# Optimization experiments

Hardware: AMD Instinct MI355X
Metric: run time of the kernel (lower is better)

The kernel has to match this reference:

```python
import jax, jax.numpy as jnp
import numpy as np

DIM = 256
HEADS = 8
WIN = 64
SHIFT = 32
HIDDEN = 1024  # dim * mlp_ratio
EPS = 1e-5


def layernorm(x, g, b):
    mu = jnp.mean(x, axis=-1, keepdims=True)
    var = jnp.mean(jnp.square(x - mu), axis=-1, keepdims=True)
    return (x - mu) * jax.lax.rsqrt(var + EPS) * g + b


def setup_inputs() -> dict:
    key = jax.random.key(0)
    ks = jax.random.split(key, 12)
    B, L = 8, 16384
    s = lambda fan: 1.0 / np.sqrt(fan)
    return {
        "x": jax.random.normal(ks[0], (B, L, DIM), dtype=jnp.float32),
        "g1": jnp.ones((DIM,), jnp.float32),
        "b1": jnp.zeros((DIM,), jnp.float32),
        "qkv_w": jax.random.normal(ks[1], (DIM, 3 * DIM), jnp.float32) * s(DIM),
        "qkv_b": jnp.zeros((3 * DIM,), jnp.float32),
        "rpb_table": jax.random.normal(ks[2], (2 * WIN - 1, HEADS), jnp.float32) * 0.02,
        "proj_w": jax.random.normal(ks[3], (DIM, DIM), jnp.float32) * s(DIM),
        "proj_b": jnp.zeros((DIM,), jnp.float32),
        "g2": jnp.ones((DIM,), jnp.float32),
        "b2": jnp.zeros((DIM,), jnp.float32),
        "fc1_w": jax.random.normal(ks[4], (DIM, HIDDEN), jnp.float32) * s(DIM),
        "fc1_b": jnp.zeros((HIDDEN,), jnp.float32),
        "fc2_w": jax.random.normal(ks[5], (HIDDEN, DIM), jnp.float32) * s(HIDDEN),
        "fc2_b": jnp.zeros((DIM,), jnp.float32),
    }


def reference(x, g1, b1, qkv_w, qkv_b, rpb_table, proj_w, proj_b, g2, b2, fc1_w, fc1_b, fc2_w, fc2_b):
    B, L, C = x.shape
    hd = C // HEADS
    scale = hd ** (-0.5)

    shortcut = x
    xn = layernorm(x, g1, b1)

    # shift: roll left, zero wrapped-around tail (faithful to original in-place zeroing)
    shifted = jnp.roll(xn, -SHIFT, axis=1)
    shifted = shifted.at[:, -SHIFT:].set(0.0)

    nW = L // WIN
    xw = shifted.reshape(B * nW, WIN, C)

    # qkv projection
    qkv = xw @ qkv_w + qkv_b
    qkv = qkv.reshape(-1, WIN, 3, HEADS, hd).transpose(2, 0, 3, 1, 4)
    q, k, v = qkv[0], qkv[1], qkv[2]

    attn = jnp.einsum('bhnd,bhmd->bhnm', q * scale, k)

    idx = jnp.arange(WIN)
    rel = idx[:, None] - idx[None, :] + (WIN - 1)
    bias = rpb_table[rel].transpose(2, 0, 1)
    attn = attn + bias[None]

    attn = jax.nn.softmax(attn, axis=-1)
    out = jnp.einsum('bhnm,bhmd->bhnd', attn, v)
    out = out.transpose(0, 2, 1, 3).reshape(-1, WIN, C)
    out = out @ proj_w + proj_b

    # window reverse + unshift (zero wrapped head, faithful to original)
    xr = out.reshape(B, L, C)
    xr = jnp.roll(xr, SHIFT, axis=1)
    xr = xr.at[:, :SHIFT].set(0.0)

    x1 = shortcut + xr
    h = layernorm(x1, g2, b2)
    h = jax.nn.gelu(h @ fc1_w + fc1_b, approximate=False)
    h = h @ fc2_w + fc2_b
    return x1 + h
```

## Files before the change

### kernel.cpp

```cpp
#include <hip/hip_runtime.h>
#include <hip/hip_bf16.h>
#include <stdint.h>

#define LSEQ   16384
#define NBATCH 8
#define MROWS  (NBATCH*LSEQ)
#define CDIM   256
#define NHEADS 8
#define HDIM   32
#define NWIN   64
#define NSH    32
#define NHID   1024

typedef unsigned short u16;
typedef __attribute__((ext_vector_type(4))) float f32x4;
typedef __attribute__((ext_vector_type(8))) short s16x8;

__device__ __forceinline__ u16 f2bf(float f) {
  union { float f; unsigned u; } c; c.f = f;
  unsigned r = c.u + 0x7FFFu + ((c.u >> 16) & 1u);
  return (u16)(r >> 16);
}

__device__ __forceinline__ float gelu_fast(float v) {
  float t = v * v;
  float u2 = v * fmaf(t, 0.0713548162726f, 1.59576912161f);
  float e = __expf(u2);
  float r = __builtin_amdgcn_rcpf(e + 1.f);
  return fmaf(-v, r, v);
}

__global__ __launch_bounds__(256) void wtrans_kernel(const float* __restrict__ in,
                                                     u16* __restrict__ out, int K, int N) {
  __shared__ float tile[64][65];
  int k0 = blockIdx.x * 64, n0 = blockIdx.y * 64;
  int t = threadIdx.x;
  int r = t >> 4, cb = (t & 15) * 4;
#pragma unroll
  for (int p = 0; p < 4; ++p) {
    const float4 v = *(const float4*)(in + (size_t)(k0 + r + p*16) * N + n0 + cb);
    tile[r+p*16][cb+0] = v.x; tile[r+p*16][cb+1] = v.y;
    tile[r+p*16][cb+2] = v.z; tile[r+p*16][cb+3] = v.w;
  }
  __syncthreads();
#pragma unroll
  for (int p = 0; p < 4; ++p) {
    int nl = r + p*16;
    ushort4 o;
    o.x = f2bf(tile[cb+0][nl]); o.y = f2bf(tile[cb+1][nl]);
    o.z = f2bf(tile[cb+2][nl]); o.w = f2bf(tile[cb+3][nl]);
    *(ushort4*)(out + (size_t)(n0+nl)*K + k0 + cb) = o;
  }
}

__global__ __launch_bounds__(256) void ln_shift_kernel(const float* __restrict__ x,
                                                       const float* __restrict__ g,
                                                       const float* __restrict__ b,
                                                       u16* __restrict__ out) {
  int row  = blockIdx.x * 4 + (threadIdx.x >> 6);
  int lane = threadIdx.x & 63;
  u16* op = out + (size_t)row * CDIM + lane*4;
  int l  = row & (LSEQ-1);
  int ls = l + NSH;
  if (ls >= LSEQ) { *(ushort4*)op = make_ushort4(0,0,0,0); return; }
  const float4 v = *(const float4*)(x + ((size_t)(row - l) + ls) * CDIM + lane*4);
  float s  = v.x+v.y+v.z+v.w;
  float s2 = v.x*v.x + v.y*v.y + v.z*v.z + v.w*v.w;
#pragma unroll
  for (int m = 1; m < 64; m <<= 1) { s += __shfl_xor(s, m); s2 += __shfl_xor(s2, m); }
  float mean = s * (1.f/CDIM);
  float rs = rsqrtf(s2*(1.f/CDIM) - mean*mean + 1e-5f);
  const float4 gv = *(const float4*)(g + lane*4);
  const float4 bv = *(const float4*)(b + lane*4);
  ushort4 o;
  o.x = f2bf((v.x-mean)*rs*gv.x + bv.x);
  o.y = f2bf((v.y-mean)*rs*gv.y + bv.y);
  o.z = f2bf((v.z-mean)*rs*gv.z + bv.z);
  o.w = f2bf((v.w-mean)*rs*gv.w + bv.w);
  *(ushort4*)op = o;
}

template<int KDIM, int NDIM, int EPI>
__global__ __launch_bounds__(256) void gemm_kernel(const u16* __restrict__ A,
                                                   const u16* __restrict__ BT,
                                                   const float* __restrict__ bias,
                                                   void* __restrict__ Cout,
                                                   const float* __restrict__ res) {
  __shared__ __align__(16) u16 As[128*64];
  __shared__ __align__(16) u16 Bs[128*64];
  const int t = threadIdx.x, wave = t >> 6, lane = t & 63;
  constexpr int NT_N = NDIM / 128;
  constexpr int G = 32;
  const int bid = blockIdx.x;
  const int chunk = bid / (G * NT_N);
  const int rem = bid - chunk * (G * NT_N);
  const int tn = rem / G;
  const int tm = chunk * G + (rem - tn * G);
  f32x4 acc[4][4];
#pragma unroll
  for (int m = 0; m < 4; ++m)
#pragma unroll
    for (int n = 0; n < 4; ++n) acc[m][n] = (f32x4){0.f,0.f,0.f,0.f};

  const size_t Aoff = (size_t)tm * 128 * KDIM;
  const size_t Boff = (size_t)tn * 128 * KDIM;
  int rowS[4], kblkS[4];
#pragma unroll
  for (int p = 0; p < 4; ++p) {
    int i = p*256 + t; rowS[p] = i >> 3;
    kblkS[p] = ((i & 7) ^ (rowS[p] & 7)) * 8;
  }
  const int wr = (wave >> 1) * 64, wc = (wave & 1) * 64;

  for (int kt = 0; kt < KDIM/64; ++kt) {
    const int k0 = kt * 64;
#pragma unroll
    for (int p = 0; p < 4; ++p) {
      __builtin_amdgcn_global_load_lds(
        (const __attribute__((address_space(1))) void*)(A + Aoff + (size_t)rowS[p]*KDIM + k0 + kblkS[p]),
        (__attribute__((address_space(3))) void*)(As + (p*256 + wave*64)*8), 16, 0, 0);
      __builtin_amdgcn_global_load_lds(
        (const __attribute__((address_space(1))) void*)(BT + Boff + (size_t)rowS[p]*KDIM + k0 + kblkS[p]),
        (__attribute__((address_space(3))) void*)(Bs + (p*256 + wave*64)*8), 16, 0, 0);
    }
    asm volatile("s_waitcnt vmcnt(0)" ::: "memory");
    __syncthreads();
#pragma unroll
    for (int kk = 0; kk < 2; ++kk) {
      s16x8 af[4], bf[4];
#pragma unroll
      for (int m = 0; m < 4; ++m) {
        int r = wr + m*16 + (lane & 15);
        int slot = (kk*4 + (lane >> 4)) ^ (r & 7);
        af[m] = *(const s16x8*)&As[r*64 + slot*8];
      }
#pragma unroll
      for (int n = 0; n < 4; ++n) {
        int r = wc + n*16 + (lane & 15);
        int slot = (kk*4 + (lane >> 4)) ^ (r & 7);
        bf[n] = *(const s16x8*)&Bs[r*64 + slot*8];
      }
#pragma unroll
      for (int m = 0; m < 4; ++m)
#pragma unroll
        for (int n = 0; n < 4; ++n)
          acc[m][n] = __builtin_amdgcn_mfma_f32_16x16x32_bf16(bf[n], af[m], acc[m][n], 0, 0, 0);
    }
    __syncthreads();
  }

  const int g = lane >> 4, c0 = lane & 15;
  const size_t row0 = (size_t)tm*128 + wr;
  const int col0 = tn*128 + wc;
  float4 bvv[4];
#pragma unroll
  for (int n = 0; n < 4; ++n) bvv[n] = *(const float4*)(bias + col0 + n*16 + g*4);

  if constexpr (EPI == 0) {
    u16* out = (u16*)Cout;
#pragma unroll
    for (int m = 0; m < 4; ++m) {
      size_t R = row0 + m*16 + c0;
      u16* orow = out + R * NDIM + col0 + g*4;
#pragma unroll
      for (int n = 0; n < 4; ++n) {
        ushort4 o;
        o.x = f2bf(acc[m][n][0] + bvv[n].x);
        o.y = f2bf(acc[m][n][1] + bvv[n].y);
        o.z = f2bf(acc[m][n][2] + bvv[n].z);
        o.w = f2bf(acc[m][n][3] + bvv[n].w);
        *(ushort4*)(orow + n*16) = o;
      }
    }
  } else if constexpr (EPI == 2) {
    u16* out = (u16*)Cout;
#pragma unroll
    for (int m = 0; m < 4; ++m) {
      size_t R = row0 + m*16 + c0;
      u16* orow = out + R * NDIM + col0 + g*4;
#pragma unroll
      for (int n = 0; n < 4; ++n) {
        ushort4 o;
        o.x = f2bf(gelu_fast(acc[m][n][0] + bvv[n].x));
        o.y = f2bf(gelu_fast(acc[m][n][1] + bvv[n].y));
        o.z = f2bf(gelu_fast(acc[m][n][2] + bvv[n].z));
        o.w = f2bf(gelu_fast(acc[m][n][3] + bvv[n].w));
        *(ushort4*)(orow + n*16) = o;
      }
    }
  } else {
    float* out = (float*)Cout;
#pragma unroll
    for (int m = 0; m < 4; ++m) {
      size_t R = row0 + m*16 + c0;
      size_t base = R * NDIM + col0 + g*4;
#pragma unroll
      for (int n = 0; n < 4; ++n) {
        float4 rv = *(const float4*)(res + base + n*16);
        float4 o;
        o.x = rv.x + acc[m][n][0] + bvv[n].x;
        o.y = rv.y + acc[m][n][1] + bvv[n].y;
        o.z = rv.z + acc[m][n][2] + bvv[n].z;
        o.w = rv.w + acc[m][n][3] + bvv[n].w;
        *(float4*)(out + base + n*16) = o;
      }
    }
  }
}

__global__ __launch_bounds__(256) void proj_ln_kernel(const u16* __restrict__ A,
                                                      const u16* __restrict__ BT,
                                                      const float* __restrict__ bias,
                                                      const float* __restrict__ x,
                                                      const float* __restrict__ g2,
                                                      const float* __restrict__ b2,
                                                      float* __restrict__ out,
                                                      u16* __restrict__ ln_out) {
  __shared__ __align__(16) u16 As[64*64];
  __shared__ __align__(16) u16 Bs[256*64];
  const int t = threadIdx.x, wave = t >> 6, lane = t & 63;
  const int g = lane >> 4, c0 = lane & 15;
  const int row0 = blockIdx.x * 64;

  f32x4 acc[16];
#pragma unroll
  for (int n = 0; n < 16; ++n) acc[n] = (f32x4){0.f,0.f,0.f,0.f};

  for (int kt = 0; kt < 4; ++kt) {
    const int k0 = kt * 64;
#pragma unroll
    for (int p = 0; p < 2; ++p) {
      int i = p*256 + t;
      int r = i >> 3;
      int srow = row0 - NSH + r; if (srow < 0) srow = 0;
      int kb = ((i & 7) ^ (r & 7)) * 8;
      __builtin_amdgcn_global_load_lds(
        (const __attribute__((address_space(1))) void*)(A + (size_t)srow*CDIM + k0 + kb),
        (__attribute__((address_space(3))) void*)(As + i*8), 16, 0, 0);
    }
#pragma unroll
    for (int p = 0; p < 8; ++p) {
      int i = p*256 + t;
      int r = i >> 3;
      int kb = ((i & 7) ^ (r & 7)) * 8;
      __builtin_amdgcn_global_load_lds(
        (const __attribute__((address_space(1))) void*)(BT + (size_t)r*CDIM + k0 + kb),
        (__attribute__((address_space(3))) void*)(Bs + i*8), 16, 0, 0);
    }
    asm volatile("s_waitcnt vmcnt(0)" ::: "memory");
    __syncthreads();
#pragma unroll
    for (int kk = 0; kk < 2; ++kk) {
      const int ar = wave*16 + c0;
      s16x8 af = *(const s16x8*)&As[ar*64 + (((kk*4 + g) ^ (ar & 7)) * 8)];
#pragma unroll
      for (int nn = 0; nn < 4; ++nn) {
        s16x8 bf[4];
#pragma unroll
        for (int q = 0; q < 4; ++q) {
          int rn = (nn*4 + q)*16 + c0;
          bf[q] = *(const s16x8*)&Bs[rn*64 + (((kk*4 + g) ^ (rn & 7)) * 8)];
        }
#pragma unroll
        for (int q = 0; q < 4; ++q)
          acc[nn*4+q] = __builtin_amdgcn_mfma_f32_16x16x32_bf16(bf[q], af, acc[nn*4+q], 0, 0, 0);
      }
    }
    __syncthreads();
  }

  const int D = row0 + wave*16 + c0;
  const int l_d = D & (LSEQ-1);
  const bool addp = (l_d >= NSH);
  float s = 0.f, s2 = 0.f;
  f32x4 x1v[16];
#pragma unroll
  for (int n = 0; n < 16; ++n) {
    const int col = n*16 + g*4;
    const float4 xv = *(const float4*)(x + (size_t)D*CDIM + col);
    const float4 bv = *(const float4*)(bias + col);
    f32x4 v;
    v[0] = addp ? xv.x + acc[n][0] + bv.x : xv.x;
    v[1] = addp ? xv.y + acc[n][1] + bv.y : xv.y;
    v[2] = addp ? xv.z + acc[n][2] + bv.z : xv.z;
    v[3] = addp ? xv.w + acc[n][3] + bv.w : xv.w;
    *(f32x4*)(out + (size_t)D*CDIM + col) = v;
    x1v[n] = v;
    s  += v[0]+v[1]+v[2]+v[3];
    s2 += v[0]*v[0]+v[1]*v[1]+v[2]*v[2]+v[3]*v[3];
  }
  s  += __shfl_xor(s, 16);  s  += __shfl_xor(s, 32);
  s2 += __shfl_xor(s2, 16); s2 += __shfl_xor(s2, 32);
  const float mean = s * (1.f/CDIM);
  const float rs = rsqrtf(s2*(1.f/CDIM) - mean*mean + 1e-5f);
#pragma unroll
  for (int n = 0; n < 16; ++n) {
    const int col = n*16 + g*4;
    const float4 gv = *(const float4*)(g2 + col);
    const float4 bv = *(const float4*)(b2 + col);
    ushort4 o;
    o.x = f2bf((x1v[n][0]-mean)*rs*gv.x + bv.x);
    o.y = f2bf((x1v[n][1]-mean)*rs*gv.y + bv.y);
    o.z = f2bf((x1v[n][2]-mean)*rs*gv.z + bv.z);
    o.w = f2bf((x1v[n][3]-mean)*rs*gv.w + bv.w);
    *(ushort4*)(ln_out + (size_t)D*CDIM + col) = o;
  }
}

__global__ __launch_bounds__(256) void attn_kernel(const u16* __restrict__ qkv,
                                                   const float* __restrict__ rpb,
                                                   u16* __restrict__ out) {
  __shared__ __align__(16) u16 VT[NHEADS*HDIM*NWIN];
  __shared__ __align__(16) u16 Pl[4*NWIN*NWIN];
  __shared__ float biasl[NHEADS][128];
  const int t = threadIdx.x, wave = t >> 6, lane = t & 63;
  const int g = lane >> 4, c0 = lane & 15;
  const size_t rowbase = (size_t)blockIdx.x * NWIN;

  for (int e = t; e < NHEADS*128; e += 256) {
    int h = e >> 7, i = e & 127;
    biasl[h][i] = (i < 2*NWIN-1) ? rpb[i*NHEADS + h] : 0.f;
  }
  {
    int cA = t >> 5;
    int inner = t & 31;
    int hh = inner >> 2, d0 = (inner & 3) * 8;
#pragma unroll
    for (int p = 0; p < 8; ++p) {
      int c = p*8 + cA;
      s16x8 v = *(const s16x8*)&qkv[(rowbase + c)*768 + 512 + hh*32 + d0];
#pragma unroll
      for (int j = 0; j < 8; ++j) {
        int d = d0 + j;
        int slot = (c >> 3) ^ (d & 7) ^ hh;
        *(u16*)((char*)VT + hh*4096 + d*128 + slot*16 + (c & 7)*2) = (u16)v[j];
      }
    }
  }
  __syncthreads();

  const float scale = 0.17677669529663687f;
#pragma unroll 1
  for (int rep = 0; rep < 2; ++rep) {
    const int h = wave*2 + rep;
    s16x8 qf[4], kf[4];
#pragma unroll
    for (int m = 0; m < 4; ++m)
      qf[m] = *(const s16x8*)&qkv[(rowbase + m*16 + c0)*768 + h*32 + g*8];
#pragma unroll
    for (int n = 0; n < 4; ++n)
      kf[n] = *(const s16x8*)&qkv[(rowbase + n*16 + c0)*768 + 256 + h*32 + g*8];
    f32x4 sa[4][4];
#pragma unroll
    for (int m = 0; m < 4; ++m)
#pragma unroll
      for (int n = 0; n < 4; ++n) sa[m][n] = (f32x4){0.f,0.f,0.f,0.f};
#pragma unroll
    for (int m = 0; m < 4; ++m)
#pragma unroll
      for (int n = 0; n < 4; ++n)
        sa[m][n] = __builtin_amdgcn_mfma_f32_16x16x32_bf16(qf[m], kf[n], sa[m][n], 0, 0, 0);
#pragma unroll
    for (int m = 0; m < 4; ++m)
#pragma unroll
      for (int n = 0; n < 4; ++n) {
        int idx0 = (m-n)*16 + 4*g - c0 + 63;
#pragma unroll
        for (int j = 0; j < 4; ++j)
          sa[m][n][j] = sa[m][n][j]*scale + biasl[h][idx0 + j];
      }
    float rm[4][4], rsum[4][4];
#pragma unroll
    for (int m = 0; m < 4; ++m)
#pragma unroll
      for (int j = 0; j < 4; ++j) {
        float mx = fmaxf(fmaxf(sa[m][0][j], sa[m][1][j]), fmaxf(sa[m][2][j], sa[m][3][j]));
        mx = fmaxf(mx, __shfl_xor(mx, 1));
        mx = fmaxf(mx, __shfl_xor(mx, 2));
        mx = fmaxf(mx, __shfl_xor(mx, 4));
        mx = fmaxf(mx, __shfl_xor(mx, 8));
        rm[m][j] = mx;
      }
#pragma unroll
    for (int m = 0; m < 4; ++m)
#pragma unroll
      for (int n = 0; n < 4; ++n)
#pragma unroll
        for (int j = 0; j < 4; ++j)
          sa[m][n][j] = __expf(sa[m][n][j] - rm[m][j]);
#pragma unroll
    for (int m = 0; m < 4; ++m)
#pragma unroll
      for (int j = 0; j < 4; ++j) {
        float s = sa[m][0][j] + sa[m][1][j] + sa[m][2][j] + sa[m][3][j];
        s += __shfl_xor(s, 1);
        s += __shfl_xor(s, 2);
        s += __shfl_xor(s, 4);
        s += __shfl_xor(s, 8);
        rsum[m][j] = 1.f / s;
      }
    asm volatile("s_waitcnt lgkmcnt(0)" ::: "memory");
#pragma unroll
    for (int m = 0; m < 4; ++m)
#pragma unroll
      for (int n = 0; n < 4; ++n)
#pragma unroll
        for (int j = 0; j < 4; ++j) {
          int r = m*16 + 4*g + j, c = n*16 + c0;
          *(u16*)((char*)Pl + wave*8192 + r*128 + (((c>>3)^(r&7))*16) + (c&7)*2)
            = f2bf(sa[m][n][j] * rsum[m][j]);
        }
    asm volatile("s_waitcnt lgkmcnt(0)" ::: "memory");
    __builtin_amdgcn_sched_barrier(0);
    f32x4 oa[4][2];
#pragma unroll
    for (int m = 0; m < 4; ++m) { oa[m][0] = (f32x4){0.f,0.f,0.f,0.f}; oa[m][1] = (f32x4){0.f,0.f,0.f,0.f}; }
#pragma unroll
    for (int kk = 0; kk < 2; ++kk) {
      s16x8 pa[4], vb[2];
#pragma unroll
      for (int m = 0; m < 4; ++m) {
        int r = m*16 + c0;
        int slot = (kk*4 + g) ^ (r & 7);
        pa[m] = *(const s16x8*)((const char*)Pl + wave*8192 + r*128 + slot*16);
      }
#pragma unroll
      for (int n = 0; n < 2; ++n) {
        int d = n*16 + c0;
        int slot = (kk*4 + g) ^ (d & 7) ^ h;
        vb[n] = *(const s16x8*)((const char*)VT + h*4096 + d*128 + slot*16);
      }
#pragma unroll
      for (int m = 0; m < 4; ++m)
#pragma unroll
        for (int n = 0; n < 2; ++n)
          oa[m][n] = __builtin_amdgcn_mfma_f32_16x16x32_bf16(vb[n], pa[m], oa[m][n], 0, 0, 0);
    }
#pragma unroll
    for (int m = 0; m < 4; ++m) {
      u16* op = out + (rowbase + m*16 + c0)*CDIM + h*32 + g*4;
#pragma unroll
      for (int n = 0; n < 2; ++n) {
        ushort4 o;
        o.x = f2bf(oa[m][n][0]); o.y = f2bf(oa[m][n][1]);
        o.z = f2bf(oa[m][n][2]); o.w = f2bf(oa[m][n][3]);
        *(ushort4*)(op + n*16) = o;
      }
    }
  }
}

extern "C" void kernel_launch(void* const* d_in, const int* in_sizes, int n_in,
                              void* d_out, int out_size, void* d_ws, size_t ws_size,
                              hipStream_t stream) {
  const float* x      = (const float*)d_in[0];
  const float* g1     = (const float*)d_in[1];
  const float* b1     = (const float*)d_in[2];
  const float* qkv_w  = (const float*)d_in[3];
  const float* qkv_b  = (const float*)d_in[4];
  const float* rpb    = (const float*)d_in[5];
  const float* proj_w = (const float*)d_in[6];
  const float* proj_b = (const float*)d_in[7];
  const float* g2     = (const float*)d_in[8];
  const float* b2     = (const float*)d_in[9];
  const float* fc1_w  = (const float*)d_in[10];
  const float* fc1_b  = (const float*)d_in[11];
  const float* fc2_w  = (const float*)d_in[12];
  const float* fc2_b  = (const float*)d_in[13];
  float* out = (float*)d_out;

  u16* R0     = (u16*)d_ws;
  u16* R1     = R0 + (size_t)MROWS*768;
  u16* qkvwT  = R1 + (size_t)MROWS*1024;
  u16* projwT = qkvwT + 768*256;
  u16* fc1wT  = projwT + 256*256;
  u16* fc2wT  = fc1wT + 1024*256;

  wtrans_kernel<<<dim3(4, 12), 256, 0, stream>>>(qkv_w, qkvwT, 256, 768);
  wtrans_kernel<<<dim3(4, 4),  256, 0, stream>>>(proj_w, projwT, 256, 256);
  wtrans_kernel<<<dim3(4, 16), 256, 0, stream>>>(fc1_w, fc1wT, 256, 1024);
  wtrans_kernel<<<dim3(16, 4), 256, 0, stream>>>(fc2_w, fc2wT, 1024, 256);

  constexpr int NT_M = MROWS/128;
  ln_shift_kernel<<<MROWS/4, 256, 0, stream>>>(x, g1, b1, R1);
  gemm_kernel<256, 768, 0><<<NT_M*6, 256, 0, stream>>>(R1, qkvwT, qkv_b, R0, nullptr);
  attn_kernel<<<MROWS/NWIN, 256, 0, stream>>>(R0, rpb, R1);
  proj_ln_kernel<<<MROWS/64, 256, 0, stream>>>(R1, projwT, proj_b, x, g2, b2, out, R0);
  gemm_kernel<256, 1024, 2><<<NT_M*8, 256, 0, stream>>>(R0, fc1wT, fc1_b, R1, nullptr);
  gemm_kernel<1024, 256, 3><<<NT_M*2, 256, 0, stream>>>(R1, fc2wT, fc2_b, out, out);
}
```

Baseline: 682.4 us.

## Double-buffer LDS tiles in GEMM and proj kernels to overlap loads with MFMA

Converts the generic GEMM and the fused proj+LayerNorm kernel from a single-buffered load-wait-compute loop into a two-stage ping-pong. The next K tile is fetched into a second LDS buffer with global_load_lds while MFMAs run on the current one, which hides global memory latency. LDS use doubles, which may lower occupancy. The block-swizzle group size is also reduced for large-K GEMMs (the fc2 GEMM) to change L2 reuse.

```diff
diff --git a/kernel.cpp b/kernel.cpp
--- a/kernel.cpp
+++ b/kernel.cpp
@@ -86,11 +86,12 @@
                                                    const float* __restrict__ bias,
                                                    void* __restrict__ Cout,
                                                    const float* __restrict__ res) {
-  __shared__ __align__(16) u16 As[128*64];
-  __shared__ __align__(16) u16 Bs[128*64];
+  __shared__ __align__(16) u16 As[2][128*64];
+  __shared__ __align__(16) u16 Bs[2][128*64];
   const int t = threadIdx.x, wave = t >> 6, lane = t & 63;
   constexpr int NT_N = NDIM / 128;
-  constexpr int G = 32;
+  constexpr int G = (KDIM >= 1024) ? 8 : 32;
+  constexpr int NTK = KDIM / 64;
   const int bid = blockIdx.x;
   const int chunk = bid / (G * NT_N);
   const int rem = bid - chunk * (G * NT_N);
@@ -112,19 +113,19 @@
   }
   const int wr = (wave >> 1) * 64, wc = (wave & 1) * 64;
 
-  for (int kt = 0; kt < KDIM/64; ++kt) {
+  auto STAGE = [&](u16* AsD, u16* BsD, int kt) {
     const int k0 = kt * 64;
 #pragma unroll
     for (int p = 0; p < 4; ++p) {
       __builtin_amdgcn_global_load_lds(
         (const __attribute__((address_space(1))) void*)(A + Aoff + (size_t)rowS[p]*KDIM + k0 + kblkS[p]),
-        (__attribute__((address_space(3))) void*)(As + (p*256 + wave*64)*8), 16, 0, 0);
+        (__attribute__((address_space(3))) void*)(AsD + (p*256 + wave*64)*8), 16, 0, 0);
       __builtin_amdgcn_global_load_lds(
         (const __attribute__((address_space(1))) void*)(BT + Boff + (size_t)rowS[p]*KDIM + k0 + kblkS[p]),
-        (__attribute__((address_space(3))) void*)(Bs + (p*256 + wave*64)*8), 16, 0, 0);
-    }
-    asm volatile("s_waitcnt vmcnt(0)" ::: "memory");
-    __syncthreads();
+        (__attribute__((address_space(3))) void*)(BsD + (p*256 + wave*64)*8), 16, 0, 0);
+    }
+  };
+  auto COMPUTE = [&](const u16* AsS, const u16* BsS) {
 #pragma unroll
     for (int kk = 0; kk < 2; ++kk) {
       s16x8 af[4], bf[4];
@@ -132,13 +133,13 @@
       for (int m = 0; m < 4; ++m) {
         int r = wr + m*16 + (lane & 15);
         int slot = (kk*4 + (lane >> 4)) ^ (r & 7);
-        af[m] = *(const s16x8*)&As[r*64 + slot*8];
+        af[m] = *(const s16x8*)&AsS[r*64 + slot*8];
       }
 #pragma unroll
       for (int n = 0; n < 4; ++n) {
         int r = wc + n*16 + (lane & 15);
         int slot = (kk*4 + (lane >> 4)) ^ (r & 7);
-        bf[n] = *(const s16x8*)&Bs[r*64 + slot*8];
+        bf[n] = *(const s16x8*)&BsS[r*64 + slot*8];
       }
 #pragma unroll
       for (int m = 0; m < 4; ++m)
@@ -146,6 +147,21 @@
         for (int n = 0; n < 4; ++n)
           acc[m][n] = __builtin_amdgcn_mfma_f32_16x16x32_bf16(bf[n], af[m], acc[m][n], 0, 0, 0);
     }
+  };
+
+  STAGE(As[0], Bs[0], 0);
+  asm volatile("s_waitcnt vmcnt(0)" ::: "memory");
+  __syncthreads();
+#pragma unroll 1
+  for (int kt2 = 0; kt2 < NTK/2; ++kt2) {
+    const int kt = kt2 * 2;
+    if (kt + 1 < NTK) STAGE(As[1], Bs[1], kt + 1);
+    COMPUTE(As[0], Bs[0]);
+    asm volatile("s_waitcnt vmcnt(0)" ::: "memory");
+    __syncthreads();
+    if (kt + 2 < NTK) STAGE(As[0], Bs[0], kt + 2);
+    COMPUTE(As[1], Bs[1]);
+    asm volatile("s_waitcnt vmcnt(0)" ::: "memory");
     __syncthreads();
   }
 
@@ -216,8 +232,8 @@
                                                       const float* __restrict__ b2,
                                                       float* __restrict__ out,
                                                       u16* __restrict__ ln_out) {
-  __shared__ __align__(16) u16 As[64*64];
-  __shared__ __align__(16) u16 Bs[256*64];
+  __shared__ __align__(16) u16 As[2][64*64];
+  __shared__ __align__(16) u16 Bs[2][256*64];
   const int t = threadIdx.x, wave = t >> 6, lane = t & 63;
   const int g = lane >> 4, c0 = lane & 15;
   const int row0 = blockIdx.x * 64;
@@ -226,7 +242,7 @@
 #pragma unroll
   for (int n = 0; n < 16; ++n) acc[n] = (f32x4){0.f,0.f,0.f,0.f};
 
-  for (int kt = 0; kt < 4; ++kt) {
+  auto STAGE = [&](u16* AsD, u16* BsD, int kt) {
     const int k0 = kt * 64;
 #pragma unroll
     for (int p = 0; p < 2; ++p) {
@@ -236,7 +252,7 @@
       int kb = ((i & 7) ^ (r & 7)) * 8;
       __builtin_amdgcn_global_load_lds(
         (const __attribute__((address_space(1))) void*)(A + (size_t)srow*CDIM + k0 + kb),
-        (__attribute__((address_space(3))) void*)(As + i*8), 16, 0, 0);
+        (__attribute__((address_space(3))) void*)(AsD + i*8), 16, 0, 0);
     }
 #pragma unroll
     for (int p = 0; p < 8; ++p) {
@@ -245,27 +261,42 @@
       int kb = ((i & 7) ^ (r & 7)) * 8;
       __builtin_amdgcn_global_load_lds(
         (const __attribute__((address_space(1))) void*)(BT + (size_t)r*CDIM + k0 + kb),
-        (__attribute__((address_space(3))) void*)(Bs + i*8), 16, 0, 0);
-    }
+        (__attribute__((address_space(3))) void*)(BsD + i*8), 16, 0, 0);
+    }
+  };
+  auto COMPUTE = [&](const u16* AsS, const u16* BsS) {
+#pragma unroll
+    for (int kk = 0; kk < 2; ++kk) {
+      const int ar = wave*16 + c0;
+      s16x8 af = *(const s16x8*)&AsS[ar*64 + (((kk*4 + g) ^ (ar & 7)) * 8)];
+#pragma unroll
+      for (int nn = 0; nn < 4; ++nn) {
+        s16x8 bf[4];
+#pragma unroll
+        for (int q = 0; q < 4; ++q) {
+          int rn = (nn*4 + q)*16 + c0;
+          bf[q] = *(const s16x8*)&BsS[rn*64 + (((kk*4 + g) ^ (rn & 7)) * 8)];
+        }
+#pragma unroll
+        for (int q = 0; q < 4; ++q)
+          acc[nn*4+q] = __builtin_amdgcn_mfma_f32_16x16x32_bf16(bf[q], af, acc[nn*4+q], 0, 0, 0);
+      }
+    }
+  };
+
+  STAGE(As[0], Bs[0], 0);
+  asm volatile("s_waitcnt vmcnt(0)" ::: "memory");
+  __syncthreads();
+#pragma unroll 1
+  for (int kt2 = 0; kt2 < 2; ++kt2) {
+    const int kt = kt2 * 2;
+    if (kt + 1 < 4) STAGE(As[1], Bs[1], kt + 1);
+    COMPUTE(As[0], Bs[0]);
     asm volatile("s_waitcnt vmcnt(0)" ::: "memory");
     __syncthreads();
-#pragma unroll
-    for (int kk = 0; kk < 2; ++kk) {
-      const int ar = wave*16 + c0;
-      s16x8 af = *(const s16x8*)&As[ar*64 + (((kk*4 + g) ^ (ar & 7)) * 8)];
-#pragma unroll
-      for (int nn = 0; nn < 4; ++nn) {
-        s16x8 bf[4];
-#pragma unroll
-        for (int q = 0; q < 4; ++q) {
-          int rn = (nn*4 + q)*16 + c0;
-          bf[q] = *(const s16x8*)&Bs[rn*64 + (((kk*4 + g) ^ (rn & 7)) * 8)];
-        }
-#pragma unroll
-        for (int q = 0; q < 4; ++q)
-          acc[nn*4+q] = __builtin_amdgcn_mfma_f32_16x16x32_bf16(bf[q], af, acc[nn*4+q], 0, 0, 0);
-      }
-    }
+    if (kt + 2 < 4) STAGE(As[0], Bs[0], kt + 2);
+    COMPUTE(As[1], Bs[1]);
+    asm volatile("s_waitcnt vmcnt(0)" ::: "memory");
     __syncthreads();
   }
 
```

Measured after the change: 741.0 us. 1.09x slower.

## Fuse fc1, GELU and fc2 into one MLP kernel keeping hidden activations in LDS

Applied to the files above, without the earlier changes.

Replaces the two separate MLP GEMM launches with a single kernel. Each block processes 64 rows: it keeps the normalized input tile in LDS, computes the hidden layer in 128-column chunks with GELU into LDS, and immediately accumulates the fc2 product, then adds the residual. This removes the global write and re-read of the 128K x 1024 bf16 hidden activation. In exchange, weights are reloaded per block with no double buffering, tiles are smaller, and the loads are fully synchronous, so MFMA utilization may drop.

```diff
diff --git a/kernel.cpp b/kernel.cpp
--- a/kernel.cpp
+++ b/kernel.cpp
@@ -80,12 +80,11 @@
   *(ushort4*)op = o;
 }
 
-template<int KDIM, int NDIM, int EPI>
+template<int KDIM, int NDIM>
 __global__ __launch_bounds__(256) void gemm_kernel(const u16* __restrict__ A,
                                                    const u16* __restrict__ BT,
                                                    const float* __restrict__ bias,
-                                                   void* __restrict__ Cout,
-                                                   const float* __restrict__ res) {
+                                                   u16* __restrict__ Cout) {
   __shared__ __align__(16) u16 As[128*64];
   __shared__ __align__(16) u16 Bs[128*64];
   const int t = threadIdx.x, wave = t >> 6, lane = t & 63;
@@ -155,55 +154,18 @@
   float4 bvv[4];
 #pragma unroll
   for (int n = 0; n < 4; ++n) bvv[n] = *(const float4*)(bias + col0 + n*16 + g*4);
-
-  if constexpr (EPI == 0) {
-    u16* out = (u16*)Cout;
-#pragma unroll
-    for (int m = 0; m < 4; ++m) {
-      size_t R = row0 + m*16 + c0;
-      u16* orow = out + R * NDIM + col0 + g*4;
-#pragma unroll
-      for (int n = 0; n < 4; ++n) {
-        ushort4 o;
-        o.x = f2bf(acc[m][n][0] + bvv[n].x);
-        o.y = f2bf(acc[m][n][1] + bvv[n].y);
-        o.z = f2bf(acc[m][n][2] + bvv[n].z);
-        o.w = f2bf(acc[m][n][3] + bvv[n].w);
-        *(ushort4*)(orow + n*16) = o;
-      }
-    }
-  } else if constexpr (EPI == 2) {
-    u16* out = (u16*)Cout;
-#pragma unroll
-    for (int m = 0; m < 4; ++m) {
-      size_t R = row0 + m*16 + c0;
-      u16* orow = out + R * NDIM + col0 + g*4;
-#pragma unroll
-      for (int n = 0; n < 4; ++n) {
-        ushort4 o;
-        o.x = f2bf(gelu_fast(acc[m][n][0] + bvv[n].x));
-        o.y = f2bf(gelu_fast(acc[m][n][1] + bvv[n].y));
-        o.z = f2bf(gelu_fast(acc[m][n][2] + bvv[n].z));
-        o.w = f2bf(gelu_fast(acc[m][n][3] + bvv[n].w));
-        *(ushort4*)(orow + n*16) = o;
-      }
-    }
-  } else {
-    float* out = (float*)Cout;
-#pragma unroll
-    for (int m = 0; m < 4; ++m) {
-      size_t R = row0 + m*16 + c0;
-      size_t base = R * NDIM + col0 + g*4;
-#pragma unroll
-      for (int n = 0; n < 4; ++n) {
-        float4 rv = *(const float4*)(res + base + n*16);
-        float4 o;
-        o.x = rv.x + acc[m][n][0] + bvv[n].x;
-        o.y = rv.y + acc[m][n][1] + bvv[n].y;
-        o.z = rv.z + acc[m][n][2] + bvv[n].z;
-        o.w = rv.w + acc[m][n][3] + bvv[n].w;
-        *(float4*)(out + base + n*16) = o;
-      }
+#pragma unroll
+  for (int m = 0; m < 4; ++m) {
+    size_t R = row0 + m*16 + c0;
+    u16* orow = Cout + R * NDIM + col0 + g*4;
+#pragma unroll
+    for (int n = 0; n < 4; ++n) {
+      ushort4 o;
+      o.x = f2bf(acc[m][n][0] + bvv[n].x);
+      o.y = f2bf(acc[m][n][1] + bvv[n].y);
+      o.z = f2bf(acc[m][n][2] + bvv[n].z);
+      o.w = f2bf(acc[m][n][3] + bvv[n].w);
+      *(ushort4*)(orow + n*16) = o;
     }
   }
 }
@@ -304,6 +266,145 @@
     o.z = f2bf((x1v[n][2]-mean)*rs*gv.z + bv.z);
     o.w = f2bf((x1v[n][3]-mean)*rs*gv.w + bv.w);
     *(ushort4*)(ln_out + (size_t)D*CDIM + col) = o;
+  }
+}
+
+__global__ __launch_bounds__(256) void mlp_kernel(const u16* __restrict__ A,
+                                                  const u16* __restrict__ W1T,
+                                                  const u16* __restrict__ W2T,
+                                                  const float* __restrict__ b1,
+                                                  const float* __restrict__ b2,
+                                                  float* __restrict__ out) {
+  __shared__ __align__(16) u16 Xs[64*256];
+  __shared__ __align__(16) u16 Ws[256*64];
+  __shared__ __align__(16) u16 Hs[64*128];
+  const int t = threadIdx.x, wave = t >> 6, lane = t & 63;
+  const int g = lane >> 4, c0 = lane & 15;
+  const int row0 = blockIdx.x * 64;
+
+#pragma unroll
+  for (int p = 0; p < 8; ++p) {
+    int i = p*256 + t, r = i >> 5, cb = i & 31;
+    __builtin_amdgcn_global_load_lds(
+      (const __attribute__((address_space(1))) void*)(A + (size_t)(row0 + r)*CDIM + ((cb ^ (r & 7))*8)),
+      (__attribute__((address_space(3))) void*)(Xs + i*8), 16, 0, 0);
+  }
+  f32x4 acc2[4][4];
+#pragma unroll
+  for (int m = 0; m < 4; ++m)
+#pragma unroll
+    for (int n = 0; n < 4; ++n) acc2[m][n] = (f32x4){0.f,0.f,0.f,0.f};
+  asm volatile("s_waitcnt vmcnt(0)" ::: "memory");
+  __syncthreads();
+
+#pragma unroll 1
+  for (int hc = 0; hc < 8; ++hc) {
+    f32x4 acc1[4][2];
+#pragma unroll
+    for (int m = 0; m < 4; ++m) { acc1[m][0] = (f32x4){0.f,0.f,0.f,0.f}; acc1[m][1] = (f32x4){0.f,0.f,0.f,0.f}; }
+#pragma unroll
+    for (int kt = 0; kt < 4; ++kt) {
+#pragma unroll
+      for (int p = 0; p < 4; ++p) {
+        int i = p*256 + t, r = i >> 3, cb = i & 7;
+        __builtin_amdgcn_global_load_lds(
+          (const __attribute__((address_space(1))) void*)(W1T + (size_t)(hc*128 + r)*256 + kt*64 + ((cb ^ (r & 7))*8)),
+          (__attribute__((address_space(3))) void*)(Ws + i*8), 16, 0, 0);
+      }
+      asm volatile("s_waitcnt vmcnt(0)" ::: "memory");
+      __syncthreads();
+#pragma unroll
+      for (int kk = 0; kk < 2; ++kk) {
+        s16x8 af[4], bf[2];
+        const int q = kt*2 + kk;
+#pragma unroll
+        for (int m = 0; m < 4; ++m) {
+          int r = m*16 + c0;
+          af[m] = *(const s16x8*)&Xs[r*256 + (((q*4 + g) ^ (r & 7))*8)];
+        }
+#pragma unroll
+        for (int n = 0; n < 2; ++n) {
+          int rw = wave*32 + n*16 + c0;
+          bf[n] = *(const s16x8*)&Ws[rw*64 + (((kk*4 + g) ^ (rw & 7))*8)];
+        }
+#pragma unroll
+        for (int m = 0; m < 4; ++m)
+#pragma unroll
+          for (int n = 0; n < 2; ++n)
+            acc1[m][n] = __builtin_amdgcn_mfma_f32_16x16x32_bf16(bf[n], af[m], acc1[m][n], 0, 0, 0);
+      }
+      __syncthreads();
+    }
+    {
+      float4 b1v[2];
+#pragma unroll
+      for (int n = 0; n < 2; ++n) b1v[n] = *(const float4*)(b1 + hc*128 + wave*32 + n*16 + g*4);
+#pragma unroll
+      for (int m = 0; m < 4; ++m) {
+        int r = m*16 + c0;
+#pragma unroll
+        for (int n = 0; n < 2; ++n) {
+          ushort4 o;
+          o.x = f2bf(gelu_fast(acc1[m][n][0] + b1v[n].x));
+          o.y = f2bf(gelu_fast(acc1[m][n][1] + b1v[n].y));
+          o.z = f2bf(gelu_fast(acc1[m][n][2] + b1v[n].z));
+          o.w = f2bf(gelu_fast(acc1[m][n][3] + b1v[n].w));
+          int colb = wave*4 + n*2 + (g >> 1);
+          *(ushort4*)((char*)Hs + r*256 + ((colb ^ (r & 7)) << 4) + (g & 1)*8) = o;
+        }
+      }
+    }
+    __syncthreads();
+#pragma unroll
+    for (int kt2 = 0; kt2 < 2; ++kt2) {
+#pragma unroll
+      for (int p = 0; p < 8; ++p) {
+        int i = p*256 + t, r = i >> 3, cb = i & 7;
+        __builtin_amdgcn_global_load_lds(
+          (const __attribute__((address_space(1))) void*)(W2T + (size_t)r*NHID + hc*128 + kt2*64 + ((cb ^ (r & 7))*8)),
+          (__attribute__((address_space(3))) void*)(Ws + i*8), 16, 0, 0);
+      }
+      asm volatile("s_waitcnt vmcnt(0)" ::: "memory");
+      __syncthreads();
+#pragma unroll
+      for (int kk = 0; kk < 2; ++kk) {
+        s16x8 af[4], bf[4];
+        const int s2 = kt2*2 + kk;
+#pragma unroll
+        for (int m = 0; m < 4; ++m) {
+          int r = m*16 + c0;
+          af[m] = *(const s16x8*)&Hs[r*128 + (((s2*4 + g) ^ (r & 7))*8)];
+        }
+#pragma unroll
+        for (int n = 0; n < 4; ++n) {
+          int rw = wave*64 + n*16 + c0;
+          bf[n] = *(const s16x8*)&Ws[rw*64 + (((kk*4 + g) ^ (rw & 7))*8)];
+        }
+#pragma unroll
+        for (int m = 0; m < 4; ++m)
+#pragma unroll
+          for (int n = 0; n < 4; ++n)
+            acc2[m][n] = __builtin_amdgcn_mfma_f32_16x16x32_bf16(bf[n], af[m], acc2[m][n], 0, 0, 0);
+      }
+      __syncthreads();
+    }
+  }
+  float4 b2v[4];
+#pragma unroll
+  for (int n = 0; n < 4; ++n) b2v[n] = *(const float4*)(b2 + wave*64 + n*16 + g*4);
+#pragma unroll
+  for (int m = 0; m < 4; ++m) {
+    size_t base = (size_t)(row0 + m*16 + c0)*CDIM + wave*64 + g*4;
+#pragma unroll
+    for (int n = 0; n < 4; ++n) {
+      float4 rv = *(const float4*)(out + base + n*16);
+      float4 o;
+      o.x = rv.x + acc2[m][n][0] + b2v[n].x;
+      o.y = rv.y + acc2[m][n][1] + b2v[n].y;
+      o.z = rv.z + acc2[m][n][2] + b2v[n].z;
+      o.w = rv.w + acc2[m][n][3] + b2v[n].w;
+      *(float4*)(out + base + n*16) = o;
+    }
   }
 }
 
@@ -483,9 +584,8 @@
 
   constexpr int NT_M = MROWS/128;
   ln_shift_kernel<<<MROWS/4, 256, 0, stream>>>(x, g1, b1, R1);
-  gemm_kernel<256, 768, 0><<<NT_M*6, 256, 0, stream>>>(R1, qkvwT, qkv_b, R0, nullptr);
+  gemm_kernel<256, 768><<<NT_M*6, 256, 0, stream>>>(R1, qkvwT, qkv_b, R0);
   attn_kernel<<<MROWS/NWIN, 256, 0, stream>>>(R0, rpb, R1);
   proj_ln_kernel<<<MROWS/64, 256, 0, stream>>>(R1, projwT, proj_b, x, g2, b2, out, R0);
-  gemm_kernel<256, 1024, 2><<<NT_M*8, 256, 0, stream>>>(R0, fc1wT, fc1_b, R1, nullptr);
-  gemm_kernel<1024, 256, 3><<<NT_M*2, 256, 0, stream>>>(R1, fc2wT, fc2_b, out, out);
-}
+  mlp_kernel<<<MROWS/64, 256, 0, stream>>>(R0, fc1wT, fc2wT, fc1_b, fc2_b, out);
+}
```

Measured after the change: 642.8 us. -5.8%, faster.
